# Performance work log

Hardware: AMD Instinct MI355X
Metric: run time of the kernel (lower is better)

The kernel has to match this reference:

```python
import jax, jax.numpy as jnp
import numpy as np

H = 24  # hidden size hard-coded in TrendGRU


def setup_inputs() -> dict:
    key = jax.random.key(0)
    ks = jax.random.split(key, 7)
    B, T = 32768, 512
    s_ih = 1.0 / np.sqrt(H)
    x = jax.random.normal(ks[0], (B, T, 1), dtype=jnp.float32)
    # GRUCell params (PyTorch layout: rows ordered r, z, n)
    W_ih = jax.random.uniform(ks[1], (3 * H, 1), minval=-s_ih, maxval=s_ih, dtype=jnp.float32)
    W_hh = jax.random.uniform(ks[2], (3 * H, H), minval=-s_ih, maxval=s_ih, dtype=jnp.float32)
    b_ih = jax.random.uniform(ks[3], (3 * H,), minval=-s_ih, maxval=s_ih, dtype=jnp.float32)
    b_hh = jax.random.uniform(ks[4], (3 * H,), minval=-s_ih, maxval=s_ih, dtype=jnp.float32)
    fc_w = jax.random.uniform(ks[5], (2, H), minval=-s_ih, maxval=s_ih, dtype=jnp.float32)
    fc_b = jax.random.uniform(ks[6], (2,), minval=-s_ih, maxval=s_ih, dtype=jnp.float32)
    return {"x": x, "W_ih": W_ih, "b_ih": b_ih, "W_hh": W_hh, "b_hh": b_hh,
            "fc_w": fc_w, "fc_b": fc_b}


def _gru_scan(x, W_ih, b_ih, W_hh, b_hh):
    B = x.shape[0]
    # precompute input projections for all timesteps: (B,T,1)@(1,3H) -> (T,B,3H)
    gx = jnp.einsum('bti,gi->tbg', x, W_ih) + b_ih
    h0 = jnp.zeros((B, H), dtype=x.dtype)

    def step(h, gx_t):
        gh = h @ W_hh.T + b_hh                      # (B, 3H)
        xr, xz, xn = jnp.split(gx_t, 3, axis=-1)    # PyTorch order r, z, n
        hr, hz, hn = jnp.split(gh, 3, axis=-1)
        r = jax.nn.sigmoid(xr + hr)
        z = jax.nn.sigmoid(xz + hz)
        n = jnp.tanh(xn + r * hn)
        h_new = (1.0 - z) * n + z * h
        return h_new, None

    h_final, _ = jax.lax.scan(step, h0, gx)
    return h_final


def reference(x, W_ih, b_ih, W_hh, b_hh, fc_w, fc_b):
    h = _gru_scan(x, W_ih, b_ih, W_hh, b_hh)
    return h @ fc_w.T + fc_b  # (B, 2)
```

## Files before the change

kernel.cpp:

```cpp
#include <hip/hip_runtime.h>


#define GRU_T 512
#define FS 28

typedef __attribute__((ext_vector_type(8)))  short bf16x8;
typedef __attribute__((ext_vector_type(16))) float f32x16;

__device__ __forceinline__ float bf16hi_f(float v) {
    unsigned u = __float_as_uint(v);
    u = (u + 0x7FFFu + ((u >> 16) & 1u)) & 0xFFFF0000u;
    return __uint_as_float(u);
}
__device__ __forceinline__ unsigned bf16_rne(float v) {
    unsigned u = __float_as_uint(v);
    return (u + 0x7FFFu + ((u >> 16) & 1u)) >> 16;
}
__device__ __forceinline__ float sigf(float a) {
    return __builtin_amdgcn_rcpf(1.0f + __builtin_amdgcn_exp2f(-a));
}
__device__ __forceinline__ float tnhf(float v) {
    return fmaf(-2.0f, __builtin_amdgcn_rcpf(1.0f + __builtin_amdgcn_exp2f(v)), 1.0f);
}
__device__ __forceinline__ f32x16 mfma32(bf16x8 a, bf16x8 b, f32x16 c) {
    return __builtin_amdgcn_mfma_f32_32x32x16_bf16(a, b, c, 0, 0, 0);
}

__global__ __launch_bounds__(64) void trend_gru_r9(
    const float* __restrict__ x,
    const float* __restrict__ W_ih,
    const float* __restrict__ b_ih,
    const float* __restrict__ W_hh,
    const float* __restrict__ b_hh,
    const float* __restrict__ fc_w,
    const float* __restrict__ fc_b,
    float* __restrict__ out)
{
    const int lane = threadIdx.x;
    const int e    = lane & 31;
    const int half = lane >> 5;
    const int elem0 = blockIdx.x * 32;

    __shared__ __align__(16) float Flds[32 * FS];

    const float L2E = 1.4426950408889634f;

    bf16x8 A[3][2][2];
#pragma unroll
    for (int g = 0; g < 3; ++g) {
        const float sc = (g == 2) ? 2.0f * L2E : L2E;
        const int m = e;
        const bool valid = m < 24;
        const int R = g * 24 + (valid ? m : 0);
        const float wx = (g < 2 && valid) ? sc * W_ih[R] : 0.0f;
        const float bb = valid ? sc * ((g < 2) ? (b_ih[R] + b_hh[R]) : b_hh[R]) : 0.0f;
        const float wxh = bf16hi_f(wx), bbh = bf16hi_f(bb);
#pragma unroll
        for (int s = 0; s < 2; ++s) {
            bf16x8 fh, fl;
#pragma unroll
            for (int jj = 0; jj < 8; ++jj) {
                const int k = s * 16 + half * 8 + jj;
                float vh = 0.0f, vl = 0.0f;
                if (valid && k < 24) {
                    const float w  = sc * W_hh[R * 24 + k];
                    const float wh = bf16hi_f(w);
                    vh = wh; vl = w - wh;
                } else if (valid) {
                    if (k == 24 || k == 25)      vh = wxh;
                    else if (k == 26)            vh = wx - wxh;
                    else if (k == 27)            vh = bbh;
                    else if (k == 28)            vh = bb - bbh;
                }
                fh[jj] = (short)bf16_rne(vh);
                fl[jj] = (short)bf16_rne(vl);
            }
            A[g][s][0] = fh;
            A[g][s][1] = fl;
        }
    }

    float wn_s[12], bn_s[12];
#pragma unroll
    for (int s = 0; s < 12; ++s) {
        const int j = (s & 3) + 8 * (s >> 2) + 4 * half;
        wn_s[s] = 2.0f * L2E * W_ih[48 + j];
        bn_s[s] = 2.0f * L2E * b_ih[48 + j];
    }

    const float* xp = x + (size_t)(elem0 + e) * GRU_T;
    float xv = xp[0];

    float h[12];
#pragma unroll
    for (int s = 0; s < 12; ++s) h[s] = 0.0f;

    unsigned P[3][2];
#pragma unroll
    for (int G = 0; G < 3; ++G) { P[G][0] = 0u; P[G][1] = 0u; }

    const f32x16 z16 = {0.f,0.f,0.f,0.f,0.f,0.f,0.f,0.f,
                        0.f,0.f,0.f,0.f,0.f,0.f,0.f,0.f};

#pragma unroll 1
    for (int t = 0; t < GRU_T; ++t) {
        uint4 xq;
        {
            const unsigned uhi = bf16_rne(xv);
            const float xh = __uint_as_float(uhi << 16);
            const unsigned ulo = bf16_rne(xv - xh);
            xq.x = uhi | (ulo << 16);
            xq.y = uhi | 0x3F800000u;
            xq.z = 0x00003F80u;
            xq.w = 0u;
        }

        unsigned Q[3][2];
#pragma unroll
        for (int G = 0; G < 3; ++G) {
            Q[G][0] = __shfl_xor((int)P[G][0], 32);
            Q[G][1] = __shfl_xor((int)P[G][1], 32);
        }

        uint4 b0v, b1v;
        b0v.x = half ? Q[1][0] : P[0][0];
        b0v.y = half ? Q[1][1] : P[0][1];
        b0v.z = half ? P[1][0] : Q[0][0];
        b0v.w = half ? P[1][1] : Q[0][1];
        b1v.x = half ? xq.x : P[2][0];
        b1v.y = half ? xq.y : P[2][1];
        b1v.z = half ? xq.z : Q[2][0];
        b1v.w = half ? xq.w : Q[2][1];
        const bf16x8 B0 = *(const bf16x8*)&b0v;
        const bf16x8 B1 = *(const bf16x8*)&b1v;

        const float xnext = xp[(t + 1 < GRU_T) ? t + 1 : t];

        f32x16 aR = mfma32(A[0][0][0], B0, z16);
        aR = mfma32(A[0][0][1], B0, aR);
        aR = mfma32(A[0][1][0], B1, aR);
        aR = mfma32(A[0][1][1], B1, aR);
        f32x16 aZ = mfma32(A[1][0][0], B0, z16);
        aZ = mfma32(A[1][0][1], B0, aZ);
        aZ = mfma32(A[1][1][0], B1, aZ);
        aZ = mfma32(A[1][1][1], B1, aZ);
        f32x16 aN = mfma32(A[2][0][0], B0, z16);
        aN = mfma32(A[2][0][1], B0, aN);
        aN = mfma32(A[2][1][0], B1, aN);
        aN = mfma32(A[2][1][1], B1, aN);

#pragma unroll
        for (int G = 0; G < 3; ++G) {
            unsigned u4[4];
#pragma unroll
            for (int q = 0; q < 4; ++q) {
                const int s = G * 4 + q;
                const float rr  = sigf(aR[s]);
                const float zz  = sigf(aZ[s]);
                const float aXv = fmaf(wn_s[s], xv, bn_s[s]);
                const float nn  = tnhf(fmaf(rr, aN[s], aXv));
                const float hn  = fmaf(zz, h[s] - nn, nn);
                h[s] = hn;
                unsigned u = __float_as_uint(hn);
                u4[q] = u + 0x7FFFu + ((u >> 16) & 1u);
            }
            P[G][0] = __builtin_amdgcn_perm(u4[1], u4[0], 0x07060302u);
            P[G][1] = __builtin_amdgcn_perm(u4[3], u4[2], 0x07060302u);
        }
        xv = xnext;
    }

#pragma unroll
    for (int G = 0; G < 3; ++G) {
        float4 f4;
        f4.x = h[G * 4 + 0]; f4.y = h[G * 4 + 1];
        f4.z = h[G * 4 + 2]; f4.w = h[G * 4 + 3];
        *(float4*)(&Flds[e * FS + G * 8 + half * 4]) = f4;
    }
    __builtin_amdgcn_s_waitcnt(0);
    if (lane < 32) {
        float o0 = fc_b[0], o1 = fc_b[1];
#pragma unroll
        for (int j = 0; j < 24; ++j) {
            const float hv = Flds[lane * FS + j];
            o0 = fmaf(hv, fc_w[j],      o0);
            o1 = fmaf(hv, fc_w[24 + j], o1);
        }
        float2 o; o.x = o0; o.y = o1;
        *(float2*)(out + (size_t)(elem0 + lane) * 2) = o;
    }
}

extern "C" void kernel_launch(void* const* d_in, const int* in_sizes, int n_in,
                              void* d_out, int out_size, void* d_ws, size_t ws_size,
                              hipStream_t stream) {
    const float* x    = (const float*)d_in[0];
    const float* W_ih = (const float*)d_in[1];
    const float* b_ih = (const float*)d_in[2];
    const float* W_hh = (const float*)d_in[3];
    const float* b_hh = (const float*)d_in[4];
    const float* fc_w = (const float*)d_in[5];
    const float* fc_b = (const float*)d_in[6];
    float* out = (float*)d_out;

    const int B = in_sizes[0] / GRU_T;
    const int grid = B / 32;
    trend_gru_r9<<<grid, 64, 0, stream>>>(x, W_ih, b_ih, W_hh, b_hh,
                                          fc_w, fc_b, out);
}
```

Measured before the change: 495.3 us.

## Permute MFMA K layout to drop cross-half shuffles and batch reciprocals

```diff
diff --git a/kernel.cpp b/kernel.cpp
--- a/kernel.cpp
+++ b/kernel.cpp
@@ -16,17 +16,20 @@
     unsigned u = __float_as_uint(v);
     return (u + 0x7FFFu + ((u >> 16) & 1u)) >> 16;
 }
-__device__ __forceinline__ float sigf(float a) {
-    return __builtin_amdgcn_rcpf(1.0f + __builtin_amdgcn_exp2f(-a));
-}
-__device__ __forceinline__ float tnhf(float v) {
-    return fmaf(-2.0f, __builtin_amdgcn_rcpf(1.0f + __builtin_amdgcn_exp2f(v)), 1.0f);
-}
 __device__ __forceinline__ f32x16 mfma32(bf16x8 a, bf16x8 b, f32x16 c) {
     return __builtin_amdgcn_mfma_f32_32x32x16_bf16(a, b, c, 0, 0, 0);
 }
-
-__global__ __launch_bounds__(64) void trend_gru_r9(
+__device__ __forceinline__ void inv4(const float d0, const float d1,
+                                     const float d2, const float d3,
+                                     float* i0, float* i1, float* i2, float* i3) {
+    const float p01 = d0 * d1, p23 = d2 * d3;
+    const float r   = __builtin_amdgcn_rcpf(p01 * p23);
+    const float r01 = r * p23, r23 = r * p01;
+    *i0 = r01 * d1; *i1 = r01 * d0;
+    *i2 = r23 * d3; *i3 = r23 * d2;
+}
+
+__global__ __launch_bounds__(64) void trend_gru_r10(
     const float* __restrict__ x,
     const float* __restrict__ W_ih,
     const float* __restrict__ b_ih,
@@ -45,6 +48,11 @@
 
     const float L2E = 1.4426950408889634f;
 
+    const int pi[32] = { 0, 1, 2, 3, 8, 9,10,11,
+                         4, 5, 6, 7,12,13,14,15,
+                        16,17,18,19,24,25,29,29,
+                        20,21,22,23,26,27,28,29};
+
     bf16x8 A[3][2][2];
 #pragma unroll
     for (int g = 0; g < 3; ++g) {
@@ -61,16 +69,22 @@
 #pragma unroll
             for (int jj = 0; jj < 8; ++jj) {
                 const int k = s * 16 + half * 8 + jj;
+                const int c = pi[k];
                 float vh = 0.0f, vl = 0.0f;
-                if (valid && k < 24) {
-                    const float w  = sc * W_hh[R * 24 + k];
-                    const float wh = bf16hi_f(w);
-                    vh = wh; vl = w - wh;
-                } else if (valid) {
-                    if (k == 24 || k == 25)      vh = wxh;
-                    else if (k == 26)            vh = wx - wxh;
-                    else if (k == 27)            vh = bbh;
-                    else if (k == 28)            vh = bb - bbh;
+                if (valid) {
+                    if (c < 24) {
+                        const float w  = sc * W_hh[R * 24 + c];
+                        const float wh = bf16hi_f(w);
+                        vh = wh; vl = w - wh;
+                    } else if (c == 24) {
+                        vh = bbh;
+                    } else if (c == 25) {
+                        vh = bb - bbh;
+                    } else if (c == 26 || c == 27) {
+                        vh = wxh;
+                    } else if (c == 28) {
+                        vh = wx - wxh;
+                    }
                 }
                 fh[jj] = (short)bf16_rne(vh);
                 fl[jj] = (short)bf16_rne(vl);
@@ -104,33 +118,15 @@
 
 #pragma unroll 1
     for (int t = 0; t < GRU_T; ++t) {
-        uint4 xq;
-        {
-            const unsigned uhi = bf16_rne(xv);
-            const float xh = __uint_as_float(uhi << 16);
-            const unsigned ulo = bf16_rne(xv - xh);
-            xq.x = uhi | (ulo << 16);
-            xq.y = uhi | 0x3F800000u;
-            xq.z = 0x00003F80u;
-            xq.w = 0u;
-        }
-
-        unsigned Q[3][2];
-#pragma unroll
-        for (int G = 0; G < 3; ++G) {
-            Q[G][0] = __shfl_xor((int)P[G][0], 32);
-            Q[G][1] = __shfl_xor((int)P[G][1], 32);
-        }
+        const unsigned uhi = bf16_rne(xv);
+        const float    xh  = __uint_as_float(uhi << 16);
+        const unsigned ulo = bf16_rne(xv - xh);
+        const unsigned c2  = half ? (uhi | (ulo << 16)) : 0x3F803F80u;
+        const unsigned c3  = half ? uhi : 0u;
 
         uint4 b0v, b1v;
-        b0v.x = half ? Q[1][0] : P[0][0];
-        b0v.y = half ? Q[1][1] : P[0][1];
-        b0v.z = half ? P[1][0] : Q[0][0];
-        b0v.w = half ? P[1][1] : Q[0][1];
-        b1v.x = half ? xq.x : P[2][0];
-        b1v.y = half ? xq.y : P[2][1];
-        b1v.z = half ? xq.z : Q[2][0];
-        b1v.w = half ? xq.w : Q[2][1];
+        b0v.x = P[0][0]; b0v.y = P[0][1]; b0v.z = P[1][0]; b0v.w = P[1][1];
+        b1v.x = P[2][0]; b1v.y = P[2][1]; b1v.z = c2;      b1v.w = c3;
         const bf16x8 B0 = *(const bf16x8*)&b0v;
         const bf16x8 B1 = *(const bf16x8*)&b1v;
 
@@ -151,15 +147,35 @@
 
 #pragma unroll
         for (int G = 0; G < 3; ++G) {
-            unsigned u4[4];
+            float dR[4], dZ[4], axv[4];
 #pragma unroll
             for (int q = 0; q < 4; ++q) {
                 const int s = G * 4 + q;
-                const float rr  = sigf(aR[s]);
-                const float zz  = sigf(aZ[s]);
-                const float aXv = fmaf(wn_s[s], xv, bn_s[s]);
-                const float nn  = tnhf(fmaf(rr, aN[s], aXv));
-                const float hn  = fmaf(zz, h[s] - nn, nn);
+                dR[q]  = 1.0f + __builtin_amdgcn_exp2f(-aR[s]);
+                dZ[q]  = 1.0f + __builtin_amdgcn_exp2f(-aZ[s]);
+                axv[q] = fmaf(wn_s[s], xv, bn_s[s]);
+            }
+            float iR[4], iZ[4];
+            inv4(dR[0], dR[1], dR[2], dR[3], &iR[0], &iR[1], &iR[2], &iR[3]);
+            inv4(dZ[0], dZ[1], dZ[2], dZ[3], &iZ[0], &iZ[1], &iZ[2], &iZ[3]);
+
+            float dN[4];
+#pragma unroll
+            for (int q = 0; q < 4; ++q) {
+                const int s = G * 4 + q;
+                float np = fmaf(iR[q], aN[s], axv[q]);
+                np = fminf(np, 30.0f);
+                dN[q] = 1.0f + __builtin_amdgcn_exp2f(np);
+            }
+            float iN[4];
+            inv4(dN[0], dN[1], dN[2], dN[3], &iN[0], &iN[1], &iN[2], &iN[3]);
+
+            unsigned u4[4];
+#pragma unroll
+            for (int q = 0; q < 4; ++q) {
+                const int s = G * 4 + q;
+                const float nn = fmaf(-2.0f, iN[q], 1.0f);
+                const float hn = fmaf(iZ[q], h[s] - nn, nn);
                 h[s] = hn;
                 unsigned u = __float_as_uint(hn);
                 u4[q] = u + 0x7FFFu + ((u >> 16) & 1u);
@@ -205,6 +221,6 @@
 
     const int B = in_sizes[0] / GRU_T;
     const int grid = B / 32;
-    trend_gru_r9<<<grid, 64, 0, stream>>>(x, W_ih, b_ih, W_hh, b_hh,
-                                          fc_w, fc_b, out);
-}
+    trend_gru_r10<<<grid, 64, 0, stream>>>(x, W_ih, b_ih, W_hh, b_hh,
+                                           fc_w, fc_b, out);
+}
```

New measurement: 524.1 us. 5.8% more time.
